# Kernel tuning notes

Hardware: AMD Instinct MI355X
Metric: run time of the kernel (lower is better)

Reference implementation:

```python
import jax, jax.numpy as jnp
import numpy as np

EMBED_DIM = 512
NUM_HEADS = 8
HEAD_DIM = EMBED_DIM // NUM_HEADS
SCALE = HEAD_DIM ** -0.5
TEMP = 1.0


def setup_inputs() -> dict:
    key = jax.random.key(0)
    ks = jax.random.split(key, 12)
    B, N, Nk, C = 4, 2048, 2048, EMBED_DIM
    s = C ** -0.5
    return {
        "x": jax.random.normal(ks[0], (B, N, C), jnp.float32),
        "y": jax.random.normal(ks[1], (B, Nk, C), jnp.float32),
        "z": jax.random.normal(ks[2], (B, Nk, C), jnp.float32),
        "Wq": jax.random.normal(ks[3], (C, C), jnp.float32) * s,
        "bq": jnp.zeros((C,), jnp.float32),
        "Wk": jax.random.normal(ks[4], (C, C), jnp.float32) * s,
        "bk": jnp.zeros((C,), jnp.float32),
        "Wv": jax.random.normal(ks[5], (C, C), jnp.float32) * s,
        "bv": jnp.zeros((C,), jnp.float32),
        "Wo": jax.random.normal(ks[6], (C, C), jnp.float32) * s,
        "bo": jnp.zeros((C,), jnp.float32),
    }


def reference(x, y, z, Wq, bq, Wk, bk, Wv, bv, Wo, bo):
    B, N, C = x.shape
    Nk = y.shape[1]
    H, D = NUM_HEADS, HEAD_DIM

    def split_heads(t, L):
        return t.reshape(B, L, H, D).transpose(0, 2, 1, 3)  # [B,H,L,D]

    q = split_heads(x @ Wq.T + bq, N)
    k = split_heads(y @ Wk.T + bk, Nk)
    v = split_heads(z @ Wv.T + bv, Nk)

    # [B,H,N,Nk] logits, scaled
    logits = jnp.einsum("bhnd,bhkd->bhnk", q, k) * SCALE

    # Gumbel-softmax (soft, tau=TEMP) with a fixed noise key
    gkey = jax.random.key(42)
    gumbels = jax.random.gumbel(gkey, logits.shape, logits.dtype)
    attn = jax.nn.softmax((logits + gumbels) / TEMP, axis=-1)

    out = jnp.einsum("bhnk,bhkd->bhnd", attn, v)
    out = out.transpose(0, 2, 1, 3).reshape(B, N, C)
    return out @ Wo.T + bo
```

## Files before the change

### kernel.cpp

```cpp
#include <hip/hip_runtime.h>
#include <hip/hip_bf16.h>
#include <stdint.h>

#define Bdim 4
#define Hdim 8
#define Ndim 2048
#define Cdim 512
#define Ddim 64
#define SCALE_F 0.125f
#define KSPLIT 4
#define LOG2E 1.44269504f
#define QSCALE_F (SCALE_F * LOG2E)

typedef __bf16 bf16_t;
typedef __bf16 bf16x8 __attribute__((ext_vector_type(8)));
typedef float f32x4 __attribute__((ext_vector_type(4)));

__device__ __forceinline__ void gumbel_tile(uint32_t base, float (&pf)[4][4]) {
  const uint32_t k1 = 42u, k2 = 0x1BD11BDAu ^ 42u;
  uint32_t s0[16], s1[16];
#pragma unroll
  for (int i = 0; i < 16; i++) {
    s0[i] = 0u;
    s1[i] = base + ((uint32_t)(i >> 2) << 11) + (uint32_t)((i & 3) * 16);
  }
#define TF_RND(rot)                                                    \
  {                                                                    \
    _Pragma("unroll") for (int i = 0; i < 16; i++) {                   \
      s0[i] += s1[i];                                                  \
      s1[i] = __builtin_rotateleft32(s1[i], (rot)) ^ s0[i];            \
    }                                                                  \
  }
#define TF_INJ(a, b)                                                   \
  {                                                                    \
    _Pragma("unroll") for (int i = 0; i < 16; i++) {                   \
      s0[i] += (a);                                                    \
      s1[i] += (b);                                                    \
    }                                                                  \
  }
#define TF_INJ1(b)                                                     \
  {                                                                    \
    _Pragma("unroll") for (int i = 0; i < 16; i++) { s1[i] += (b); }   \
  }
  TF_RND(13) TF_RND(15) TF_RND(26) TF_RND(6)
  TF_INJ(k1, k2 + 1u)
  TF_RND(17) TF_RND(29) TF_RND(16) TF_RND(24)
  TF_INJ(k2, 2u)
  TF_RND(13) TF_RND(15) TF_RND(26) TF_RND(6)
  TF_INJ1(k1 + 3u)
  TF_RND(17) TF_RND(29) TF_RND(16) TF_RND(24)
  TF_INJ(k1, k2 + 4u)
  TF_RND(13) TF_RND(15) TF_RND(26) TF_RND(6)
  TF_INJ(k2, 5u)
#undef TF_RND
#undef TF_INJ
#undef TF_INJ1
#pragma unroll
  for (int i = 0; i < 16; i++) {
    uint32_t bits = s0[i] ^ s1[i];
    uint32_t mant;
    asm("v_alignbit_b32 %0, %1, %2, 9" : "=v"(mant) : "s"(127u), "v"(bits));
    float u = __uint_as_float(mant) - 1.0f;
    pf[i >> 2][i & 3] = -__builtin_amdgcn_rcpf(__builtin_amdgcn_logf(u));
  }
}

__device__ __forceinline__ void stage8_f32(bf16_t* dst, const float* src) {
  float4 a0 = *(const float4*)src;
  float4 a1 = *(const float4*)(src + 4);
  union { bf16_t h[8]; uint4 u; } pk;
  pk.h[0] = (bf16_t)a0.x; pk.h[1] = (bf16_t)a0.y;
  pk.h[2] = (bf16_t)a0.z; pk.h[3] = (bf16_t)a0.w;
  pk.h[4] = (bf16_t)a1.x; pk.h[5] = (bf16_t)a1.y;
  pk.h[6] = (bf16_t)a1.z; pk.h[7] = (bf16_t)a1.w;
  *(uint4*)dst = pk.u;
}

template <bool AF32, bool WF32>
__device__ __forceinline__ void gemm_core_t(const void* __restrict__ Av,
                                            const void* __restrict__ Wv,
                                            int m0, int n0,
                                            bf16_t* As, bf16_t* Ws,
                                            f32x4 (&acc)[4][4]) {
  const int t = threadIdx.x;
  const int wave = t >> 6, lane = t & 63;
  const int ln = lane & 15, qd = lane >> 4;
  const int wm = wave >> 1, wn = wave & 1;

#pragma unroll
  for (int i = 0; i < 4; i++)
#pragma unroll
    for (int j = 0; j < 4; j++) acc[i][j] = (f32x4){0.f, 0.f, 0.f, 0.f};

  for (int kt = 0; kt < Cdim / 64; ++kt) {
#pragma unroll
    for (int it = 0; it < 4; ++it) {
      int vec = it * 256 + t;
      int row = vec >> 3, c8 = (vec & 7) * 8;
      if constexpr (AF32)
        stage8_f32(&As[row * 72 + c8],
                   (const float*)Av + (size_t)(m0 + row) * Cdim + kt * 64 + c8);
      else
        *(bf16x8*)&As[row * 72 + c8] =
            *((const bf16x8*)Av + ((size_t)(m0 + row) * Cdim + kt * 64 + c8) / 8);
      if constexpr (WF32)
        stage8_f32(&Ws[row * 72 + c8],
                   (const float*)Wv + (size_t)(n0 + row) * Cdim + kt * 64 + c8);
      else
        *(bf16x8*)&Ws[row * 72 + c8] =
            *((const bf16x8*)Wv + ((size_t)(n0 + row) * Cdim + kt * 64 + c8) / 8);
    }
    __syncthreads();
#pragma unroll
    for (int ks = 0; ks < 2; ++ks) {
      bf16x8 af[4], bfr[4];
#pragma unroll
      for (int i = 0; i < 4; i++)
        af[i] = *(const bf16x8*)&As[(wm * 64 + i * 16 + ln) * 72 + ks * 32 + qd * 8];
#pragma unroll
      for (int j = 0; j < 4; j++)
        bfr[j] = *(const bf16x8*)&Ws[(wn * 64 + j * 16 + ln) * 72 + ks * 32 + qd * 8];
#pragma unroll
      for (int i = 0; i < 4; i++)
#pragma unroll
        for (int j = 0; j < 4; j++)
          acc[i][j] = __builtin_amdgcn_mfma_f32_16x16x32_bf16(af[i], bfr[j],
                                                              acc[i][j], 0, 0, 0);
    }
    __syncthreads();
  }
}

__global__ __launch_bounds__(256, 3)
void qkv_gemm_kernel(const float* __restrict__ x, const float* __restrict__ y,
                     const float* __restrict__ z, const float* __restrict__ Wq,
                     const float* __restrict__ Wk, const float* __restrict__ Wv,
                     const float* __restrict__ bq, const float* __restrict__ bk,
                     const float* __restrict__ bv, bf16_t* __restrict__ qo,
                     bf16_t* __restrict__ ko, bf16_t* __restrict__ vo) {
  __shared__ bf16_t As[128 * 72];
  __shared__ bf16_t Ws[128 * 72];
  const int sel = blockIdx.z;
  const float* A = sel == 0 ? x : (sel == 1 ? y : z);
  const float* W = sel == 0 ? Wq : (sel == 1 ? Wk : Wv);
  const float* bias = sel == 0 ? bq : (sel == 1 ? bk : bv);
  bf16_t* O = sel == 0 ? qo : (sel == 1 ? ko : vo);
  const float mul = sel == 0 ? QSCALE_F : 1.0f;
  const int m0 = blockIdx.y * 128, n0 = blockIdx.x * 128;

  f32x4 acc[4][4];
  gemm_core_t<true, true>(A, W, m0, n0, As, Ws, acc);

  const int t = threadIdx.x;
  const int wave = t >> 6, lane = t & 63;
  const int ln = lane & 15, qd = lane >> 4;
  const int wm = wave >> 1, wn = wave & 1;
#pragma unroll
  for (int i = 0; i < 4; i++)
#pragma unroll
    for (int j = 0; j < 4; j++)
#pragma unroll
      for (int r = 0; r < 4; r++) {
        int grow = m0 + wm * 64 + i * 16 + qd * 4 + r;
        int gcol = n0 + wn * 64 + j * 16 + ln;
        float val = (acc[i][j][r] + bias[gcol]) * mul;
        int b = grow >> 11, n = grow & 2047;
        int h = gcol >> 6, d = gcol & 63;
        O[(((size_t)b * Hdim + h) * Ndim + n) * Ddim + d] = (bf16_t)val;
      }
}

__global__ __launch_bounds__(256, 4)
void out_gemm_kernel(const bf16_t* __restrict__ part_o,
                     const float* __restrict__ part_l,
                     const float* __restrict__ Wo,
                     const float* __restrict__ bo, float* __restrict__ out) {
  __shared__ bf16_t As[128 * 72];
  __shared__ bf16_t Ws[64 * 72];
  const int t = threadIdx.x;
  const int wave = t >> 6, lane = t & 63;
  const int ln = lane & 15, qd = lane >> 4;
  const int wm = wave >> 1, wn = wave & 1;
  const int m0 = blockIdx.y * 128, n0 = blockIdx.x * 64;

  f32x4 acc[4][2];
#pragma unroll
  for (int i = 0; i < 4; i++)
#pragma unroll
    for (int j = 0; j < 2; j++) acc[i][j] = (f32x4){0.f, 0.f, 0.f, 0.f};

  for (int kt = 0; kt < Cdim / 64; ++kt) {
#pragma unroll
    for (int it = 0; it < 4; ++it) {
      int vec = it * 256 + t;
      int row = vec >> 3, c8 = (vec & 7) * 8;
      int grow = m0 + row;
      int b = grow >> 11, n = grow & 2047;
      int qtile = n >> 6, r64 = n & 63;
      int blk = (((b * Hdim + kt) << 5) | qtile) * KSPLIT;
      const bf16_t* po = part_o + (size_t)blk * 4096 + r64 * 64 + c8;
      float l = part_l[(size_t)blk * 64 + r64] +
                part_l[(size_t)(blk + 1) * 64 + r64] +
                part_l[(size_t)(blk + 2) * 64 + r64] +
                part_l[(size_t)(blk + 3) * 64 + r64];
      float linv = 1.0f / l;
      float a8[8] = {0.f, 0.f, 0.f, 0.f, 0.f, 0.f, 0.f, 0.f};
#pragma unroll
      for (int zz = 0; zz < KSPLIT; zz++) {
        bf16x8 v = *(const bf16x8*)(po + (size_t)zz * 4096);
#pragma unroll
        for (int i = 0; i < 8; i++) a8[i] += (float)v[i];
      }
      union { bf16_t h[8]; uint4 u; } pk;
#pragma unroll
      for (int i = 0; i < 8; i++) pk.h[i] = (bf16_t)(a8[i] * linv);
      *(uint4*)&As[row * 72 + c8] = pk.u;
    }
#pragma unroll
    for (int it = 0; it < 2; ++it) {
      int vec = it * 256 + t;
      int row = vec >> 3, c8 = (vec & 7) * 8;
      stage8_f32(&Ws[row * 72 + c8],
                 Wo + (size_t)(n0 + row) * Cdim + kt * 64 + c8);
    }
    __syncthreads();
#pragma unroll
    for (int ks = 0; ks < 2; ++ks) {
      bf16x8 af[4], bfr[2];
#pragma unroll
      for (int i = 0; i < 4; i++)
        af[i] = *(const bf16x8*)&As[(wm * 64 + i * 16 + ln) * 72 + ks * 32 + qd * 8];
#pragma unroll
      for (int j = 0; j < 2; j++)
        bfr[j] = *(const bf16x8*)&Ws[(wn * 32 + j * 16 + ln) * 72 + ks * 32 + qd * 8];
#pragma unroll
      for (int i = 0; i < 4; i++)
#pragma unroll
        for (int j = 0; j < 2; j++)
          acc[i][j] = __builtin_amdgcn_mfma_f32_16x16x32_bf16(af[i], bfr[j],
                                                              acc[i][j], 0, 0, 0);
    }
    __syncthreads();
  }

#pragma unroll
  for (int i = 0; i < 4; i++)
#pragma unroll
    for (int j = 0; j < 2; j++)
#pragma unroll
      for (int r = 0; r < 4; r++) {
        int grow = m0 + wm * 64 + i * 16 + qd * 4 + r;
        int gcol = n0 + wn * 32 + j * 16 + ln;
        out[(size_t)grow * Cdim + gcol] = acc[i][j][r] + bo[gcol];
      }
}

__global__ __launch_bounds__(256, 6)
void attn_kernel(const bf16_t* __restrict__ qb, const bf16_t* __restrict__ kb,
                 const bf16_t* __restrict__ vb, bf16_t* __restrict__ part_o,
                 float* __restrict__ part_l) {
  __shared__ bf16_t Ks[64 * 72];
  __shared__ bf16_t Vt[64 * 72];
  __shared__ bf16_t Ps[64 * 72];

  const int t = threadIdx.x;
  const int wave = t >> 6, lane = t & 63;
  const int ln = lane & 15, qd = lane >> 4;
  const int qtile = blockIdx.x;
  const int bh = blockIdx.y;
  const int z = blockIdx.z;
  const int qbase = qtile * 64;
  const int kt_lo = z * (Ndim / 64 / KSPLIT);
  const int kt_hi = kt_lo + (Ndim / 64 / KSPLIT);

  const bf16_t* Qg = qb + (size_t)bh * Ndim * Ddim;
  const bf16_t* Kg = kb + (size_t)bh * Ndim * Ddim;
  const bf16_t* Vg = vb + (size_t)bh * Ndim * Ddim;

  const bf16_t* Qrow = Qg + (size_t)(qbase + wave * 16 + ln) * Ddim;
  bf16x8 qf0 = *(const bf16x8*)&Qrow[qd * 8];
  bf16x8 qf1 = *(const bf16x8*)&Qrow[32 + qd * 8];

  const bf16_t one_h = (bf16_t)1.0f;
  bf16x8 ones;
#pragma unroll
  for (int i = 0; i < 8; i++) ones[i] = one_h;

  const int row0 = t >> 3,        c80 = (t & 7) * 8;
  const int row1 = (256 + t) >> 3, c81 = ((256 + t) & 7) * 8;
  const int swz0 = ((row0 >> 3) ^ (c80 >> 3)) * 8 + (row0 & 7);
  const int swz1 = ((row1 >> 3) ^ (c81 >> 3)) * 8 + (row1 & 7);

  bf16x8 kr0 = *(const bf16x8*)&Kg[(size_t)(kt_lo * 64 + row0) * Ddim + c80];
  bf16x8 kr1 = *(const bf16x8*)&Kg[(size_t)(kt_lo * 64 + row1) * Ddim + c81];
  bf16x8 vr0 = *(const bf16x8*)&Vg[(size_t)(kt_lo * 64 + row0) * Ddim + c80];
  bf16x8 vr1 = *(const bf16x8*)&Vg[(size_t)(kt_lo * 64 + row1) * Ddim + c81];

  f32x4 l_acc = (f32x4){0.f, 0.f, 0.f, 0.f};
  f32x4 o_acc[4];
#pragma unroll
  for (int j = 0; j < 4; j++) o_acc[j] = (f32x4){0.f, 0.f, 0.f, 0.f};

  const uint32_t base_rc = ((uint32_t)bh << 22) +
                           ((uint32_t)(qbase + wave * 16 + qd * 4) << 11) +
                           (uint32_t)ln + 42u;

  float pf[4][4];
  gumbel_tile(base_rc + (uint32_t)(kt_lo * 64), pf);

  for (int kt = kt_lo; kt < kt_hi; ++kt) {
    *(bf16x8*)&Ks[row0 * 72 + c80] = kr0;
    *(bf16x8*)&Ks[row1 * 72 + c81] = kr1;
#pragma unroll
    for (int jj = 0; jj < 8; jj++) Vt[(c80 + jj) * 72 + swz0] = vr0[jj];
#pragma unroll
    for (int jj = 0; jj < 8; jj++) Vt[(c81 + jj) * 72 + swz1] = vr1[jj];
    __syncthreads();

    if (kt + 1 < kt_hi) {
      kr0 = *(const bf16x8*)&Kg[(size_t)((kt + 1) * 64 + row0) * Ddim + c80];
      kr1 = *(const bf16x8*)&Kg[(size_t)((kt + 1) * 64 + row1) * Ddim + c81];
      vr0 = *(const bf16x8*)&Vg[(size_t)((kt + 1) * 64 + row0) * Ddim + c80];
      vr1 = *(const bf16x8*)&Vg[(size_t)((kt + 1) * 64 + row1) * Ddim + c81];
    }

    f32x4 s[4];
#pragma unroll
    for (int j = 0; j < 4; j++) s[j] = (f32x4){0.f, 0.f, 0.f, 0.f};
#pragma unroll
    for (int j = 0; j < 4; j++) {
      bf16x8 bk0 = *(const bf16x8*)&Ks[(j * 16 + ln) * 72 + qd * 8];
      bf16x8 bk1 = *(const bf16x8*)&Ks[(j * 16 + ln) * 72 + 32 + qd * 8];
      s[j] = __builtin_amdgcn_mfma_f32_16x16x32_bf16(qf0, bk0, s[j], 0, 0, 0);
      s[j] = __builtin_amdgcn_mfma_f32_16x16x32_bf16(qf1, bk1, s[j], 0, 0, 0);
    }

#pragma unroll
    for (int r = 0; r < 4; r++)
#pragma unroll
      for (int j = 0; j < 4; j++) {
        float pv = __builtin_amdgcn_exp2f(s[j][r]) * pf[r][j];
        Ps[(wave * 16 + qd * 4 + r) * 72 + j * 16 + ln] = (bf16_t)pv;
      }

#pragma unroll
    for (int ks = 0; ks < 2; ++ks) {
      bf16x8 af = *(const bf16x8*)&Ps[(wave * 16 + ln) * 72 + ks * 32 + qd * 8];
      l_acc = __builtin_amdgcn_mfma_f32_16x16x32_bf16(af, ones, l_acc, 0, 0, 0);
#pragma unroll
      for (int j = 0; j < 4; j++) {
        int d = j * 16 + ln;
        bf16x8 bv8 = *(const bf16x8*)&Vt[d * 72 + (((ks * 4 + qd) ^ (d >> 3)) << 3)];
        o_acc[j] = __builtin_amdgcn_mfma_f32_16x16x32_bf16(af, bv8, o_acc[j], 0, 0, 0);
      }
    }

    if (kt + 1 < kt_hi)
      gumbel_tile(base_rc + (uint32_t)((kt + 1) * 64), pf);

    __syncthreads();
  }

  const int pidx = ((bh << 5) | qtile) * KSPLIT + z;
  bf16_t* po = part_o + (size_t)pidx * 64 * 64;
  float* pl = part_l + (size_t)pidx * 64;

  if (ln == 0) {
#pragma unroll
    for (int r = 0; r < 4; r++) pl[wave * 16 + qd * 4 + r] = l_acc[r];
  }
#pragma unroll
  for (int j = 0; j < 4; j++)
#pragma unroll
    for (int r = 0; r < 4; r++) {
      int row = wave * 16 + qd * 4 + r;
      int col = j * 16 + ln;
      po[row * 64 + col] = (bf16_t)o_acc[j][r];
    }
}

extern "C" void kernel_launch(void* const* d_in, const int* in_sizes, int n_in,
                              void* d_out, int out_size, void* d_ws, size_t ws_size,
                              hipStream_t stream) {
  const float* x  = (const float*)d_in[0];
  const float* y  = (const float*)d_in[1];
  const float* z  = (const float*)d_in[2];
  const float* Wq = (const float*)d_in[3];
  const float* bq = (const float*)d_in[4];
  const float* Wk = (const float*)d_in[5];
  const float* bk = (const float*)d_in[6];
  const float* Wv = (const float*)d_in[7];
  const float* bv = (const float*)d_in[8];
  const float* Wo = (const float*)d_in[9];
  const float* bo = (const float*)d_in[10];
  float* out = (float*)d_out;

  bf16_t* base = (bf16_t*)d_ws;
  const size_t NBIG = (size_t)Bdim * Ndim * Cdim;
  bf16_t* qb  = base;
  bf16_t* kb  = qb + NBIG;
  bf16_t* vb  = kb + NBIG;
  bf16_t* part_o = vb + NBIG;
  float* part_l = (float*)(part_o + (size_t)1024 * KSPLIT * 64 * 64);

  qkv_gemm_kernel<<<dim3(Cdim / 128, (Bdim * Ndim) / 128, 3), 256, 0, stream>>>(
      x, y, z, Wq, Wk, Wv, bq, bk, bv, qb, kb, vb);

  attn_kernel<<<dim3(Ndim / 64, Bdim * Hdim, KSPLIT), 256, 0, stream>>>(
      qb, kb, vb, part_o, part_l);

  out_gemm_kernel<<<dim3(Cdim / 64, (Bdim * Ndim) / 128), 256, 0, stream>>>(
      part_o, part_l, Wo, bo, out);
}
```

Measured before the change: 466.7 us.

## Remove split-K in attention and normalize output directly into token-major buffer

Attention blocks now iterate over all key tiles instead of splitting the key range four ways. Each block normalizes by the row sum itself and writes bf16 output in [B,N,C] layout, so the output GEMM loads it directly. This removes the partial-output round trip through memory and the reduction in the GEMM prologue. In exchange there are 4x fewer, longer attention blocks and a lower launch-bounds occupancy target, which may reduce latency hiding.

```diff
diff --git a/kernel.cpp b/kernel.cpp
--- a/kernel.cpp
+++ b/kernel.cpp
@@ -8,7 +8,6 @@
 #define Cdim 512
 #define Ddim 64
 #define SCALE_F 0.125f
-#define KSPLIT 4
 #define LOG2E 1.44269504f
 #define QSCALE_F (SCALE_F * LOG2E)
 
@@ -171,9 +170,7 @@
 }
 
 __global__ __launch_bounds__(256, 4)
-void out_gemm_kernel(const bf16_t* __restrict__ part_o,
-                     const float* __restrict__ part_l,
-                     const float* __restrict__ Wo,
+void out_gemm_kernel(const bf16_t* __restrict__ ab, const float* __restrict__ Wo,
                      const float* __restrict__ bo, float* __restrict__ out) {
   __shared__ bf16_t As[128 * 72];
   __shared__ bf16_t Ws[64 * 72];
@@ -194,27 +191,8 @@
     for (int it = 0; it < 4; ++it) {
       int vec = it * 256 + t;
       int row = vec >> 3, c8 = (vec & 7) * 8;
-      int grow = m0 + row;
-      int b = grow >> 11, n = grow & 2047;
-      int qtile = n >> 6, r64 = n & 63;
-      int blk = (((b * Hdim + kt) << 5) | qtile) * KSPLIT;
-      const bf16_t* po = part_o + (size_t)blk * 4096 + r64 * 64 + c8;
-      float l = part_l[(size_t)blk * 64 + r64] +
-                part_l[(size_t)(blk + 1) * 64 + r64] +
-                part_l[(size_t)(blk + 2) * 64 + r64] +
-                part_l[(size_t)(blk + 3) * 64 + r64];
-      float linv = 1.0f / l;
-      float a8[8] = {0.f, 0.f, 0.f, 0.f, 0.f, 0.f, 0.f, 0.f};
-#pragma unroll
-      for (int zz = 0; zz < KSPLIT; zz++) {
-        bf16x8 v = *(const bf16x8*)(po + (size_t)zz * 4096);
-#pragma unroll
-        for (int i = 0; i < 8; i++) a8[i] += (float)v[i];
-      }
-      union { bf16_t h[8]; uint4 u; } pk;
-#pragma unroll
-      for (int i = 0; i < 8; i++) pk.h[i] = (bf16_t)(a8[i] * linv);
-      *(uint4*)&As[row * 72 + c8] = pk.u;
+      *(bf16x8*)&As[row * 72 + c8] =
+          *(const bf16x8*)&ab[(size_t)(m0 + row) * Cdim + kt * 64 + c8];
     }
 #pragma unroll
     for (int it = 0; it < 2; ++it) {
@@ -255,10 +233,9 @@
       }
 }
 
-__global__ __launch_bounds__(256, 6)
+__global__ __launch_bounds__(256, 4)
 void attn_kernel(const bf16_t* __restrict__ qb, const bf16_t* __restrict__ kb,
-                 const bf16_t* __restrict__ vb, bf16_t* __restrict__ part_o,
-                 float* __restrict__ part_l) {
+                 const bf16_t* __restrict__ vb, bf16_t* __restrict__ ab) {
   __shared__ bf16_t Ks[64 * 72];
   __shared__ bf16_t Vt[64 * 72];
   __shared__ bf16_t Ps[64 * 72];
@@ -268,10 +245,8 @@
   const int ln = lane & 15, qd = lane >> 4;
   const int qtile = blockIdx.x;
   const int bh = blockIdx.y;
-  const int z = blockIdx.z;
   const int qbase = qtile * 64;
-  const int kt_lo = z * (Ndim / 64 / KSPLIT);
-  const int kt_hi = kt_lo + (Ndim / 64 / KSPLIT);
+  const int NT = Ndim / 64;
 
   const bf16_t* Qg = qb + (size_t)bh * Ndim * Ddim;
   const bf16_t* Kg = kb + (size_t)bh * Ndim * Ddim;
@@ -291,10 +266,10 @@
   const int swz0 = ((row0 >> 3) ^ (c80 >> 3)) * 8 + (row0 & 7);
   const int swz1 = ((row1 >> 3) ^ (c81 >> 3)) * 8 + (row1 & 7);
 
-  bf16x8 kr0 = *(const bf16x8*)&Kg[(size_t)(kt_lo * 64 + row0) * Ddim + c80];
-  bf16x8 kr1 = *(const bf16x8*)&Kg[(size_t)(kt_lo * 64 + row1) * Ddim + c81];
-  bf16x8 vr0 = *(const bf16x8*)&Vg[(size_t)(kt_lo * 64 + row0) * Ddim + c80];
-  bf16x8 vr1 = *(const bf16x8*)&Vg[(size_t)(kt_lo * 64 + row1) * Ddim + c81];
+  bf16x8 kr0 = *(const bf16x8*)&Kg[(size_t)(row0)*Ddim + c80];
+  bf16x8 kr1 = *(const bf16x8*)&Kg[(size_t)(row1)*Ddim + c81];
+  bf16x8 vr0 = *(const bf16x8*)&Vg[(size_t)(row0)*Ddim + c80];
+  bf16x8 vr1 = *(const bf16x8*)&Vg[(size_t)(row1)*Ddim + c81];
 
   f32x4 l_acc = (f32x4){0.f, 0.f, 0.f, 0.f};
   f32x4 o_acc[4];
@@ -306,9 +281,9 @@
                            (uint32_t)ln + 42u;
 
   float pf[4][4];
-  gumbel_tile(base_rc + (uint32_t)(kt_lo * 64), pf);
-
-  for (int kt = kt_lo; kt < kt_hi; ++kt) {
+  gumbel_tile(base_rc, pf);
+
+  for (int kt = 0; kt < NT; ++kt) {
     *(bf16x8*)&Ks[row0 * 72 + c80] = kr0;
     *(bf16x8*)&Ks[row1 * 72 + c81] = kr1;
 #pragma unroll
@@ -317,7 +292,7 @@
     for (int jj = 0; jj < 8; jj++) Vt[(c81 + jj) * 72 + swz1] = vr1[jj];
     __syncthreads();
 
-    if (kt + 1 < kt_hi) {
+    if (kt + 1 < NT) {
       kr0 = *(const bf16x8*)&Kg[(size_t)((kt + 1) * 64 + row0) * Ddim + c80];
       kr1 = *(const bf16x8*)&Kg[(size_t)((kt + 1) * 64 + row1) * Ddim + c81];
       vr0 = *(const bf16x8*)&Vg[(size_t)((kt + 1) * 64 + row0) * Ddim + c80];
@@ -355,28 +330,22 @@
       }
     }
 
-    if (kt + 1 < kt_hi)
+    if (kt + 1 < NT)
       gumbel_tile(base_rc + (uint32_t)((kt + 1) * 64), pf);
 
     __syncthreads();
   }
 
-  const int pidx = ((bh << 5) | qtile) * KSPLIT + z;
-  bf16_t* po = part_o + (size_t)pidx * 64 * 64;
-  float* pl = part_l + (size_t)pidx * 64;
-
-  if (ln == 0) {
-#pragma unroll
-    for (int r = 0; r < 4; r++) pl[wave * 16 + qd * 4 + r] = l_acc[r];
-  }
-#pragma unroll
-  for (int j = 0; j < 4; j++)
-#pragma unroll
-    for (int r = 0; r < 4; r++) {
-      int row = wave * 16 + qd * 4 + r;
-      int col = j * 16 + ln;
-      po[row * 64 + col] = (bf16_t)o_acc[j][r];
-    }
+  const int b = bh >> 3, h = bh & 7;
+#pragma unroll
+  for (int r = 0; r < 4; r++) {
+    const int n = qbase + wave * 16 + qd * 4 + r;
+    const float linv = 1.0f / l_acc[r];
+    bf16_t* dst = ab + ((size_t)b * Ndim + n) * Cdim + h * 64;
+#pragma unroll
+    for (int j = 0; j < 4; j++)
+      dst[j * 16 + ln] = (bf16_t)(o_acc[j][r] * linv);
+  }
 }
 
 extern "C" void kernel_launch(void* const* d_in, const int* in_sizes, int n_in,
@@ -397,18 +366,16 @@
 
   bf16_t* base = (bf16_t*)d_ws;
   const size_t NBIG = (size_t)Bdim * Ndim * Cdim;
-  bf16_t* qb  = base;
-  bf16_t* kb  = qb + NBIG;
-  bf16_t* vb  = kb + NBIG;
-  bf16_t* part_o = vb + NBIG;
-  float* part_l = (float*)(part_o + (size_t)1024 * KSPLIT * 64 * 64);
+  bf16_t* qb = base;
+  bf16_t* kb = qb + NBIG;
+  bf16_t* vb = kb + NBIG;
+  bf16_t* ab = vb + NBIG;
 
   qkv_gemm_kernel<<<dim3(Cdim / 128, (Bdim * Ndim) / 128, 3), 256, 0, stream>>>(
       x, y, z, Wq, Wk, Wv, bq, bk, bv, qb, kb, vb);
 
-  attn_kernel<<<dim3(Ndim / 64, Bdim * Hdim, KSPLIT), 256, 0, stream>>>(
-      qb, kb, vb, part_o, part_l);
+  attn_kernel<<<dim3(Ndim / 64, Bdim * Hdim), 256, 0, stream>>>(qb, kb, vb, ab);
 
   out_gemm_kernel<<<dim3(Cdim / 64, (Bdim * Ndim) / 128), 256, 0, stream>>>(
-      part_o, part_l, Wo, bo, out);
-}
+      ab, Wo, bo, out);
+}
```

Result: faster. 433.0 us (-7.2%).
